# Kernel optimization log

Measured on AMD Instinct MI355X. Metric: run time of the kernel, lower is better.

The kernel has to match this reference:

```python
import jax, jax.numpy as jnp
import numpy as np

N = 4096    # channels * n = 4 * 1024
N_IN = 1024
FC = 512


def ldr_layer(x, G, H, subd_A, subd_B, bias):
    """y = W x + bias, where W = sum_i K(A, g_i) K(B, h_i)^T and A, B are
    subdiagonal matrices with entries subd_A, subd_B (Krylov LDR fast multiply).

    Closed form: K(A, g)[i, j] = g[i-j] * c[i] / c[i-j] for i >= j (0 otherwise),
    with c = [1, cumprod(subd_A)]. This turns the multiply into FFT
    correlations/convolutions of length 2n instead of a dense n x n GEMM.
    x: (b, n); G, H: (r, n); subd_A, subd_B: (n-1,); bias: (n,).
    """
    n = x.shape[-1]
    one = jnp.ones((1,), x.dtype)
    c = jnp.concatenate([one, jnp.cumprod(subd_A)])   # (n,) cumulative subdiag products of A
    d = jnp.concatenate([one, jnp.cumprod(subd_B)])   # (n,)
    L = 2 * n
    q = H / d                                          # (r, n)
    gp = G / c                                         # (r, n)
    p = x * d                                          # (b, n)
    # u[b, r, j] = (K(B, h_r)^T x)[j] = sum_k q[r, k] * p[b, j + k]  (cross-correlation)
    Fp = jnp.fft.rfft(p, n=L)                          # (b, n+1)
    Fq = jnp.fft.rfft(q, n=L)                          # (r, n+1)
    u = jnp.fft.irfft(Fp[:, None] * jnp.conj(Fq)[None], n=L)[..., :n]  # (b, r, n)
    # out[b, i] = c[i] * sum_r (gp_r * u[b, r])_conv[i]  (causal convolution)
    Fg = jnp.fft.rfft(gp, n=L)                         # (r, n+1)
    Fu = jnp.fft.rfft(u, n=L)                          # (b, r, n+1)
    out = jnp.fft.irfft(jnp.einsum('rk,brk->bk', Fg, Fu), n=L)[:, :n]
    return c * out + bias


def setup_inputs() -> dict:
    key = jax.random.key(0)
    ks = jax.random.split(key, 14)
    std = 0.01  # params.init_stddev
    f32 = jnp.float32
    inp = {
        'x': jax.random.normal(ks[0], (128, N_IN), f32),
        'G1': std * jax.random.normal(ks[1], (48, N), f32),
        'H1': std * jax.random.normal(ks[2], (48, N), f32),
        'subd_A1': jnp.exp(0.01 * jax.random.normal(ks[3], (N - 1,), f32)),
        'subd_B1': jnp.exp(0.01 * jax.random.normal(ks[4], (N - 1,), f32)),
        'b1': std * jax.random.normal(ks[5], (N,), f32),
        'G2': std * jax.random.normal(ks[6], (16, N), f32),
        'H2': std * jax.random.normal(ks[7], (16, N), f32),
        'subd_A2': jnp.exp(0.01 * jax.random.normal(ks[8], (N - 1,), f32)),
        'subd_B2': jnp.exp(0.01 * jax.random.normal(ks[9], (N - 1,), f32)),
        'b2': std * jax.random.normal(ks[10], (N,), f32),
        'W_logits': jax.random.normal(ks[11], (10, FC), f32) / np.sqrt(FC).astype(np.float32),
        'b_logits': std * jax.random.normal(ks[12], (10,), f32),
    }
    return inp


def reference(x, G1, H1, subd_A1, subd_B1, b1, G2, H2, subd_A2, subd_B2, b2,
              W_logits, b_logits):
    bsz, n_in = x.shape
    xp = jnp.concatenate([x, jnp.zeros((bsz, N - n_in), x.dtype)], axis=-1)  # pad to channels*n
    h = jax.nn.relu(ldr_layer(xp, G1, H1, subd_A1, subd_B1, b1))
    h = jax.nn.relu(ldr_layer(h, G2, H2, subd_A2, subd_B2, b2))
    return h[:, :FC] @ W_logits.T + b_logits
```

## Files before the change

### kernel.cpp

```cpp
#include <hip/hip_runtime.h>
#include <hip/hip_bf16.h>

#define BATCH 128
#define NIN   1024
#define NFULL 4096
#define R1    48
#define R2    16
#define FCDIM 512
#define NOUT  10

#define WS_C1  0
#define WS_D1  4096
#define WS_C2  8192
#define WS_D2  12288
#define WS_Q1  16384
#define WS_GP1 (WS_Q1 + R1*NFULL)
#define WS_Q2  (WS_GP1 + R1*NFULL)
#define WS_GP2 (WS_Q2 + R2*NFULL)
#define WS_P1  (WS_GP2 + R2*NFULL)
#define WS_P2  (WS_P1 + BATCH*NIN)
#define WS_H2  (WS_P2 + BATCH*NFULL)
#define WS_PT1 (WS_H2 + BATCH*FCDIM)
#define WS_P2M (WS_PT1 + NIN*NFULL)
#define WS_CT1 (WS_P2M + FCDIM*NFULL)
#define WS_CT2 (WS_CT1 + 16*5120)
#define WS_VP1 (WS_CT2 + 8*4608)
#define WS_VP2 (WS_VP1 + 4*BATCH*NFULL)
#define WS_END (WS_VP2 + 32*BATCH*FCDIM)

#define NCH1 16
#define NCH2 8
#define CHROWS 64
#define CTLD1 5120
#define CTLD2 4608

typedef __attribute__((ext_vector_type(8))) short bf16x8;
typedef __attribute__((ext_vector_type(4))) float f32x4;

__device__ __forceinline__ unsigned short f2b(float f) {
    unsigned u = __builtin_bit_cast(unsigned, f);
    return (unsigned short)((u + 0x7fffu + ((u >> 16) & 1u)) >> 16);
}
__device__ __forceinline__ float b2f(unsigned short h) {
    unsigned u = ((unsigned)h) << 16;
    return __builtin_bit_cast(float, u);
}
#define MFMA16(a, b, c) __builtin_amdgcn_mfma_f32_16x16x32_bf16(a, b, c, 0, 0, 0)

__global__ void __launch_bounds__(256) prep_fused(
    const float* __restrict__ x, const float* __restrict__ G1,
    const float* __restrict__ H1, const float* __restrict__ G2,
    const float* __restrict__ H2, const float* __restrict__ sA1,
    const float* __restrict__ sB1, const float* __restrict__ sA2,
    const float* __restrict__ sB2, float* __restrict__ ws) {
    __shared__ float cd[4096];
    __shared__ float tot[256];
    int b = blockIdx.x, t = threadIdx.x;
    const float* src;
    int kind, r;
    if (b < 48)       { kind = 0; r = b;       src = sB1; }
    else if (b < 96)  { kind = 1; r = b - 48;  src = sA1; }
    else if (b < 112) { kind = 2; r = b - 96;  src = sB2; }
    else if (b < 128) { kind = 3; r = b - 112; src = sA2; }
    else              { kind = 4; r = b - 128; src = sB1; }
    float loc[16];
    float prod = 1.f;
#pragma unroll
    for (int u = 0; u < 16; ++u) {
        int idx = t * 16 + u;
        float e = (idx == 0) ? 1.f : src[idx - 1];
        prod *= e;
        loc[u] = prod;
    }
    tot[t] = prod;
    __syncthreads();
    for (int off = 1; off < 256; off <<= 1) {
        float v = (t >= off) ? tot[t - off] : 1.f;
        __syncthreads();
        tot[t] *= v;
        __syncthreads();
    }
    float excl = (t == 0) ? 1.f : tot[t - 1];
#pragma unroll
    for (int u = 0; u < 16; ++u) cd[t * 16 + u] = excl * loc[u];
    __syncthreads();

    if (kind == 0) {
        const float* s0 = H1 + (size_t)r * NFULL;
        float* dst = ws + WS_Q1 + (size_t)r * NFULL;
#pragma unroll
        for (int u = 0; u < 16; ++u) { int i = t + u * 256; dst[i] = s0[i] / cd[i]; }
        if (r == 0) { float* d1 = ws + WS_D1;
#pragma unroll
            for (int u = 0; u < 16; ++u) { int i = t + u * 256; d1[i] = cd[i]; } }
    } else if (kind == 1) {
        const float* s0 = G1 + (size_t)r * NFULL;
        float* dst = ws + WS_GP1 + (size_t)r * NFULL;
#pragma unroll
        for (int u = 0; u < 16; ++u) { int i = t + u * 256; dst[i] = s0[i] / cd[i]; }
        if (r == 0) { float* c1 = ws + WS_C1;
#pragma unroll
            for (int u = 0; u < 16; ++u) { int i = t + u * 256; c1[i] = cd[i]; } }
    } else if (kind == 2) {
        const float* s0 = H2 + (size_t)r * NFULL;
        float* dst = ws + WS_Q2 + (size_t)r * NFULL;
#pragma unroll
        for (int u = 0; u < 16; ++u) { int i = t + u * 256; dst[i] = s0[i] / cd[i]; }
        if (r == 0) { float* d2 = ws + WS_D2;
#pragma unroll
            for (int u = 0; u < 16; ++u) { int i = t + u * 256; d2[i] = cd[i]; } }
    } else if (kind == 3) {
        const float* s0 = G2 + (size_t)r * NFULL;
        float* dst = ws + WS_GP2 + (size_t)r * NFULL;
#pragma unroll
        for (int u = 0; u < 16; ++u) { int i = t + u * 256; dst[i] = s0[i] / cd[i]; }
        if (r == 0) { float* c2 = ws + WS_C2;
#pragma unroll
            for (int u = 0; u < 16; ++u) { int i = t + u * 256; c2[i] = cd[i]; } }
    } else {
        unsigned short* p1h = (unsigned short*)(ws + WS_P1);
        unsigned short* p1l = p1h + BATCH * NIN;
        int row0 = r * 4;
#pragma unroll
        for (int u = 0; u < 16; ++u) {
            int lin = t + u * 256;
            int row = row0 + (lin >> 10), col = lin & 1023;
            float f = x[(size_t)row * NIN + col] * cd[col];
            unsigned short h = f2b(f);
            p1h[(size_t)row * NIN + col] = h;
            p1l[(size_t)row * NIN + col] = f2b(f - b2f(h));
        }
    }
}

__global__ void __launch_bounds__(256) gemm_rank_kernel(float* __restrict__ ws) {
    const int which = blockIdx.z;
    if (which == 1 && blockIdx.y >= 8) return;
    const float* A = ws + (which == 0 ? WS_Q1  : WS_GP2);
    const float* B = ws + (which == 0 ? WS_GP1 : WS_Q2);
    float* C       = ws + (which == 0 ? WS_PT1 : WS_P2M);
    const int Kr   = which == 0 ? R1 : R2;
    __shared__ float As[R1 * 68];
    __shared__ float Bs[R1 * 68];
    int tid = threadIdx.x;
    int tx = tid & 15, ty = tid >> 4;
    int n0 = blockIdx.x * 64;
    int m0 = blockIdx.y * 64;
    int nf4 = Kr * 16;
    for (int lin = tid; lin < nf4; lin += 256) {
        int r = lin >> 4, i4 = lin & 15;
        *(float4*)&As[r * 68 + i4 * 4] = *(const float4*)&A[(size_t)r * NFULL + m0 + i4 * 4];
        *(float4*)&Bs[r * 68 + i4 * 4] = *(const float4*)&B[(size_t)r * NFULL + n0 + i4 * 4];
    }
    __syncthreads();
    float acc[4][4] = {};
#pragma unroll 8
    for (int r = 0; r < Kr; ++r) {
        float4 a4 = *(const float4*)&As[r * 68 + ty * 4];
        float4 b4 = *(const float4*)&Bs[r * 68 + tx * 4];
        acc[0][0] += a4.x * b4.x; acc[0][1] += a4.x * b4.y;
        acc[0][2] += a4.x * b4.z; acc[0][3] += a4.x * b4.w;
        acc[1][0] += a4.y * b4.x; acc[1][1] += a4.y * b4.y;
        acc[1][2] += a4.y * b4.z; acc[1][3] += a4.y * b4.w;
        acc[2][0] += a4.z * b4.x; acc[2][1] += a4.z * b4.y;
        acc[2][2] += a4.z * b4.z; acc[2][3] += a4.z * b4.w;
        acc[3][0] += a4.w * b4.x; acc[3][1] += a4.w * b4.y;
        acc[3][2] += a4.w * b4.z; acc[3][3] += a4.w * b4.w;
    }
#pragma unroll
    for (int i = 0; i < 4; ++i) {
        int m = m0 + ty * 4 + i;
        *(float4*)&C[(size_t)m * NFULL + n0 + tx * 4] =
            make_float4(acc[i][0], acc[i][1], acc[i][2], acc[i][3]);
    }
}

__global__ void diag_scan_p1(float* __restrict__ ws) {
    const int which = blockIdx.z;
    const int nch   = which == 0 ? NCH1 : NCH2;
    if (blockIdx.y >= (unsigned)nch) return;
    float* P        = ws + (which == 0 ? WS_PT1 : WS_P2M);
    float* ctot     = ws + (which == 0 ? WS_CT1 : WS_CT2);
    const int R     = which == 0 ? NIN : FCDIM;
    const int nd    = R + NFULL - 1;
    const int ctld  = which == 0 ? CTLD1 : CTLD2;
    int t = blockIdx.x * 256 + threadIdx.x;
    if (t >= nd) return;
    int doff = t - (R - 1);
    int z = blockIdx.y;
    int m0 = z * CHROWS;
    int mlo = max(m0, -doff);
    int mhi = min(m0 + CHROWS, min(NFULL - doff, R));
    float run = 0.f;
    if (mlo < mhi) {
        float* p = P + (size_t)mlo * NFULL + (mlo + doff);
        const size_t step = NFULL + 1;
        int len = mhi - mlo;
        int s = 0;
        for (; s + 16 <= len; s += 16) {
            float v[16];
#pragma unroll
            for (int u = 0; u < 16; ++u) v[u] = p[u * step];
#pragma unroll
            for (int u = 0; u < 16; ++u) { run += v[u]; v[u] = run; }
#pragma unroll
            for (int u = 0; u < 16; ++u) p[u * step] = v[u];
            p += 16 * step;
        }
        for (; s < len; ++s) { float v = *p; run += v; *p = run; p += step; }
    }
    ctot[(size_t)z * ctld + t] = run;
}

__global__ void off_prefix(float* __restrict__ ws) {
    const int which = blockIdx.z;
    float* ct      = ws + (which == 0 ? WS_CT1 : WS_CT2);
    const int ctld = which == 0 ? CTLD1 : CTLD2;
    const int nch  = which == 0 ? NCH1 : NCH2;
    int t = blockIdx.x * 256 + threadIdx.x;
    if (t >= ctld) return;
    float run = 0.f;
    for (int z = 0; z < nch; ++z) {
        float v = ct[(size_t)z * ctld + t];
        ct[(size_t)z * ctld + t] = run;
        run += v;
    }
}

#define L1_LOADA(H0, H1, L0, L1v, KS) { \
    int kk_ = kbase + (KS) * 32 + 8 * g; \
    const unsigned short* pa_ = p1h + (size_t)(mq * 32 + lm) * NIN + kk_; \
    const unsigned short* pb_ = p1l + (size_t)(mq * 32 + lm) * NIN + kk_; \
    H0 = *(const bf16x8*)pa_;  H1 = *(const bf16x8*)(pa_ + 16 * NIN); \
    L0 = *(const bf16x8*)pb_;  L1v = *(const bf16x8*)(pb_ + 16 * NIN); }

#define L1_LOADS(KS) { \
    int kg_ = kbase + (KS) * 32 + 2 * k2; \
    const float* pr_ = P1 + (size_t)kg_ * NFULL + n0 + 2 * n2; \
    float2 va_ = *(const float2*)pr_; \
    float2 vb_ = *(const float2*)(pr_ + NFULL); \
    const float* orow_ = OFF1 + (size_t)(kg_ >> 6) * CTLD1 + (1023 + n0 + 2 * n2 - kg_); \
    float om_ = orow_[-1], oc_ = orow_[0], op_ = orow_[1]; \
    f00 = va_.x + oc_; f01 = va_.y + op_; f10 = vb_.x + om_; f11 = vb_.y + oc_; }

#define L1_WRITES() { \
    unsigned short h00_ = f2b(f00), h10_ = f2b(f10), h01_ = f2b(f01), h11_ = f2b(f11); \
    int a0_ = (2 * n2) * 20 + k2; \
    Bh[a0_]      = (unsigned)h00_ | ((unsigned)h10_ << 16); \
    Bh[a0_ + 20] = (unsigned)h01_ | ((unsigned)h11_ << 16); \
    Bl[a0_]      = (unsigned)f2b(f00 - b2f(h00_)) | ((unsigned)f2b(f10 - b2f(h10_)) << 16); \
    Bl[a0_ + 20] = (unsigned)f2b(f01 - b2f(h01_)) | ((unsigned)f2b(f11 - b2f(h11_)) << 16); }

#define L1_COMPUTE(H0, H1, L0, L1v) { \
    int nb_ = (nh * 32 + lm) * 20 + 4 * g; \
    uint4 uh0_ = *(const uint4*)&Bh[nb_];       uint4 ul0_ = *(const uint4*)&Bl[nb_]; \
    uint4 uh1_ = *(const uint4*)&Bh[nb_ + 320]; uint4 ul1_ = *(const uint4*)&Bl[nb_ + 320]; \
    bf16x8 bh0_ = __builtin_bit_cast(bf16x8, uh0_), bl0_ = __builtin_bit_cast(bf16x8, ul0_); \
    bf16x8 bh1_ = __builtin_bit_cast(bf16x8, uh1_), bl1_ = __builtin_bit_cast(bf16x8, ul1_); \
    acc00 = MFMA16(H0, bh0_, acc00); acc10 = MFMA16(H1, bh0_, acc10); \
    acc01 = MFMA16(H0, bh1_, acc01); acc11 = MFMA16(H1, bh1_, acc11); \
    acc00 = MFMA16(H0, bl0_, acc00); acc10 = MFMA16(H1, bl0_, acc10); \
    acc01 = MFMA16(H0, bl1_, acc01); acc11 = MFMA16(H1, bl1_, acc11); \
    acc00 = MFMA16(L0, bh0_, acc00); acc10 = MFMA16(L1v, bh0_, acc10); \
    acc01 = MFMA16(L0, bh1_, acc01); acc11 = MFMA16(L1v, bh1_, acc11); }

#define L1_STEP(CH0, CH1, CL0, CL1, NH0, NH1, NL0, NL1, KS, LAST) \
    __syncthreads(); \
    L1_WRITES(); \
    if (!(LAST)) { L1_LOADS((KS) + 1); L1_LOADA(NH0, NH1, NL0, NL1, (KS) + 1); } \
    __syncthreads(); \
    L1_COMPUTE(CH0, CH1, CL0, CL1);

__global__ void __launch_bounds__(512)
gemm2_l1_mfma(const float* __restrict__ P1, const float* __restrict__ OFF1,
              const unsigned short* __restrict__ p1h,
              const unsigned short* __restrict__ p1l, float* __restrict__ vp) {
    __shared__ unsigned Bh[64 * 20];
    __shared__ unsigned Bl[64 * 20];
    const int t = threadIdx.x;
    const int n0 = blockIdx.x * 64;
    const int kbase = blockIdx.z * 256;
    const int w = t >> 6, l = t & 63;
    const int mq = w >> 1, nh = w & 1;
    const int lm = l & 15, g = l >> 4;
    const int k2 = t >> 5, n2 = t & 31;

    f32x4 zero = {0.f, 0.f, 0.f, 0.f};
    f32x4 acc00 = zero, acc01 = zero, acc10 = zero, acc11 = zero;
    bf16x8 ahA0, ahA1, alA0, alA1, ahB0, ahB1, alB0, alB1;
    float f00, f01, f10, f11;

    L1_LOADS(0);
    L1_LOADA(ahA0, ahA1, alA0, alA1, 0);
    L1_STEP(ahA0, ahA1, alA0, alA1, ahB0, ahB1, alB0, alB1, 0, 0)
    L1_STEP(ahB0, ahB1, alB0, alB1, ahA0, ahA1, alA0, alA1, 1, 0)
    L1_STEP(ahA0, ahA1, alA0, alA1, ahB0, ahB1, alB0, alB1, 2, 0)
    L1_STEP(ahB0, ahB1, alB0, alB1, ahA0, ahA1, alA0, alA1, 3, 0)
    L1_STEP(ahA0, ahA1, alA0, alA1, ahB0, ahB1, alB0, alB1, 4, 0)
    L1_STEP(ahB0, ahB1, alB0, alB1, ahA0, ahA1, alA0, alA1, 5, 0)
    L1_STEP(ahA0, ahA1, alA0, alA1, ahB0, ahB1, alB0, alB1, 6, 0)
    L1_STEP(ahB0, ahB1, alB0, alB1, ahA0, ahA1, alA0, alA1, 7, 1)

    float* dst = vp + (size_t)blockIdx.z * BATCH * NFULL;
    int row0 = mq * 32 + 4 * g;
    int col0 = n0 + nh * 32 + lm;
#pragma unroll
    for (int r = 0; r < 4; ++r) {
        dst[(size_t)(row0 + r) * NFULL + col0]           = acc00[r];
        dst[(size_t)(row0 + r) * NFULL + col0 + 16]      = acc01[r];
        dst[(size_t)(row0 + 16 + r) * NFULL + col0]      = acc10[r];
        dst[(size_t)(row0 + 16 + r) * NFULL + col0 + 16] = acc11[r];
    }
}

__global__ void reduce_l1_kernel(const float* __restrict__ vp, const float* __restrict__ c1,
                                 const float* __restrict__ b1, const float* __restrict__ d2,
                                 unsigned short* __restrict__ p2h,
                                 unsigned short* __restrict__ p2l) {
    int idx4 = blockIdx.x * 256 + threadIdx.x;
    int base = idx4 * 4;
    int n = base & (NFULL - 1);
    float4 s = make_float4(0.f, 0.f, 0.f, 0.f);
#pragma unroll
    for (int z = 0; z < 4; ++z) {
        float4 v = *(const float4*)&vp[(size_t)z * BATCH * NFULL + base];
        s.x += v.x; s.y += v.y; s.z += v.z; s.w += v.w;
    }
    float4 cc = *(const float4*)&c1[n];
    float4 bb = *(const float4*)&b1[n];
    float4 dd = *(const float4*)&d2[n];
    float f[4];
    f[0] = fmaxf(cc.x * s.x + bb.x, 0.f) * dd.x;
    f[1] = fmaxf(cc.y * s.y + bb.y, 0.f) * dd.y;
    f[2] = fmaxf(cc.z * s.z + bb.z, 0.f) * dd.z;
    f[3] = fmaxf(cc.w * s.w + bb.w, 0.f) * dd.w;
    ushort4 hv, lv;
    unsigned short h;
    h = f2b(f[0]); hv.x = h; lv.x = f2b(f[0] - b2f(h));
    h = f2b(f[1]); hv.y = h; lv.y = f2b(f[1] - b2f(h));
    h = f2b(f[2]); hv.z = h; lv.z = f2b(f[2] - b2f(h));
    h = f2b(f[3]); hv.w = h; lv.w = f2b(f[3] - b2f(h));
    *(ushort4*)&p2h[base] = hv;
    *(ushort4*)&p2l[base] = lv;
}

__global__ void __launch_bounds__(512)
gemm2_l2_mfma(const unsigned short* __restrict__ p2h,
              const unsigned short* __restrict__ p2l,
              const float* __restrict__ M2, const float* __restrict__ OFF2,
              float* __restrict__ vp) {
    const int t = threadIdx.x;
    const int n0 = blockIdx.x * 64;
    const int kbase = blockIdx.z * 128;
    const int w = t >> 6, l = t & 63;
    const int mq = w >> 1, nh = w & 1;
    const int lm = l & 15, g = l >> 4;
    f32x4 zero = {0.f, 0.f, 0.f, 0.f};
    f32x4 acc00 = zero, acc01 = zero, acc10 = zero, acc11 = zero;
    const int nn0 = n0 + nh * 32 + lm;
    const int nn1 = nn0 + 16;
    const float* om0 = OFF2 + (size_t)(nn0 >> 6) * CTLD2 + (511 - nn0);
    const float* om1 = OFF2 + (size_t)(nn1 >> 6) * CTLD2 + (511 - nn1);
#pragma unroll
    for (int ks = 0; ks < 4; ++ks) {
        int kk = kbase + ks * 32 + 8 * g;
        const unsigned short* pa = p2h + (size_t)(mq * 32 + lm) * NFULL + kk;
        const unsigned short* pb = p2l + (size_t)(mq * 32 + lm) * NFULL + kk;
        bf16x8 ah0 = *(const bf16x8*)pa, ah1 = *(const bf16x8*)(pa + 16 * NFULL);
        bf16x8 al0 = *(const bf16x8*)pb, al1 = *(const bf16x8*)(pb + 16 * NFULL);
        bf16x8 bh0, bl0, bh1, bl1;
        {
            const float* pm = M2 + (size_t)nn0 * NFULL + kk;
#pragma unroll
            for (int r = 0; r < 8; ++r) {
                float f = pm[r] + om0[kk + r];
                unsigned short h = f2b(f);
                bh0[r] = (short)h; bl0[r] = (short)f2b(f - b2f(h));
            }
        }
        {
            const float* pm = M2 + (size_t)nn1 * NFULL + kk;
#pragma unroll
            for (int r = 0; r < 8; ++r) {
                float f = pm[r] + om1[kk + r];
                unsigned short h = f2b(f);
                bh1[r] = (short)h; bl1[r] = (short)f2b(f - b2f(h));
            }
        }
        acc00 = MFMA16(ah0, bh0, acc00); acc10 = MFMA16(ah1, bh0, acc10);
        acc01 = MFMA16(ah0, bh1, acc01); acc11 = MFMA16(ah1, bh1, acc11);
        acc00 = MFMA16(ah0, bl0, acc00); acc10 = MFMA16(ah1, bl0, acc10);
        acc01 = MFMA16(ah0, bl1, acc01); acc11 = MFMA16(ah1, bl1, acc11);
        acc00 = MFMA16(al0, bh0, acc00); acc10 = MFMA16(al1, bh0, acc10);
        acc01 = MFMA16(al0, bh1, acc01); acc11 = MFMA16(al1, bh1, acc11);
    }
    float* dst = vp + (size_t)blockIdx.z * BATCH * FCDIM;
    int row0 = mq * 32 + 4 * g;
    int col0 = n0 + nh * 32 + lm;
#pragma unroll
    for (int r = 0; r < 4; ++r) {
        dst[(size_t)(row0 + r) * FCDIM + col0]           = acc00[r];
        dst[(size_t)(row0 + r) * FCDIM + col0 + 16]      = acc01[r];
        dst[(size_t)(row0 + 16 + r) * FCDIM + col0]      = acc10[r];
        dst[(size_t)(row0 + 16 + r) * FCDIM + col0 + 16] = acc11[r];
    }
}

__global__ void fused_out_kernel(const float* __restrict__ vp, const float* __restrict__ c2,
                                 const float* __restrict__ b2, const float* __restrict__ Wl,
                                 const float* __restrict__ bl, float* __restrict__ out) {
    __shared__ float h2s[FCDIM];
    int b = blockIdx.x, t = threadIdx.x;
    for (int col = t; col < FCDIM; col += 256) {
        float s = 0.f;
#pragma unroll
        for (int z = 0; z < 32; ++z)
            s += vp[((size_t)z * BATCH + b) * FCDIM + col];
        h2s[col] = fmaxf(c2[col] * s + b2[col], 0.f);
    }
    __syncthreads();
    int w = t >> 6, lane = t & 63;
    for (int o = w; o < NOUT; o += 4) {
        float s = 0.f;
#pragma unroll
        for (int i = lane; i < FCDIM; i += 64) s += h2s[i] * Wl[(size_t)o * FCDIM + i];
#pragma unroll
        for (int off = 32; off > 0; off >>= 1) s += __shfl_down(s, off);
        if (lane == 0) out[(size_t)b * NOUT + o] = s + bl[o];
    }
}

extern "C" void kernel_launch(void* const* d_in, const int* in_sizes, int n_in,
                              void* d_out, int out_size, void* d_ws, size_t ws_size,
                              hipStream_t stream) {
    const float* x   = (const float*)d_in[0];
    const float* G1  = (const float*)d_in[1];
    const float* H1  = (const float*)d_in[2];
    const float* sA1 = (const float*)d_in[3];
    const float* sB1 = (const float*)d_in[4];
    const float* b1  = (const float*)d_in[5];
    const float* G2  = (const float*)d_in[6];
    const float* H2  = (const float*)d_in[7];
    const float* sA2 = (const float*)d_in[8];
    const float* sB2 = (const float*)d_in[9];
    const float* b2  = (const float*)d_in[10];
    const float* Wl  = (const float*)d_in[11];
    const float* bl  = (const float*)d_in[12];
    float* out = (float*)d_out;
    float* ws = (float*)d_ws;
    (void)in_sizes; (void)n_in; (void)out_size; (void)ws_size;

    unsigned short* p1h = (unsigned short*)(ws + WS_P1);
    unsigned short* p1l = p1h + BATCH * NIN;
    unsigned short* p2h = (unsigned short*)(ws + WS_P2);
    unsigned short* p2l = p2h + BATCH * NFULL;

    prep_fused<<<160, 256, 0, stream>>>(x, G1, H1, G2, H2, sA1, sB1, sA2, sB2, ws);

    gemm_rank_kernel<<<dim3(64, 16, 2), 256, 0, stream>>>(ws);

    diag_scan_p1<<<dim3(20, NCH1, 2), 256, 0, stream>>>(ws);
    off_prefix<<<dim3(20, 1, 2), 256, 0, stream>>>(ws);

    gemm2_l1_mfma<<<dim3(64, 1, 4), 512, 0, stream>>>(ws + WS_PT1, ws + WS_CT1,
                                                      p1h, p1l, ws + WS_VP1);
    reduce_l1_kernel<<<512, 256, 0, stream>>>(ws + WS_VP1, ws + WS_C1, b1, ws + WS_D2,
                                              p2h, p2l);

    gemm2_l2_mfma<<<dim3(8, 1, 32), 512, 0, stream>>>(p2h, p2l, ws + WS_P2M,
                                                      ws + WS_CT2, ws + WS_VP2);

    fused_out_kernel<<<BATCH, 256, 0, stream>>>(ws + WS_VP2, ws + WS_C2, b2, Wl, bl, out);
}
```

Before: 70.94 us.

## Fuse rank-factor scaling into GEMM, drop layer-1 split-K, prefetch layer-2 operands

```diff
diff --git a/kernel.cpp b/kernel.cpp
--- a/kernel.cpp
+++ b/kernel.cpp
@@ -13,24 +13,18 @@
 #define WS_D1  4096
 #define WS_C2  8192
 #define WS_D2  12288
-#define WS_Q1  16384
-#define WS_GP1 (WS_Q1 + R1*NFULL)
-#define WS_Q2  (WS_GP1 + R1*NFULL)
-#define WS_GP2 (WS_Q2 + R2*NFULL)
-#define WS_P1  (WS_GP2 + R2*NFULL)
+#define WS_P1  16384
 #define WS_P2  (WS_P1 + BATCH*NIN)
-#define WS_H2  (WS_P2 + BATCH*NFULL)
-#define WS_PT1 (WS_H2 + BATCH*FCDIM)
+#define WS_PT1 (WS_P2 + BATCH*NFULL)
 #define WS_P2M (WS_PT1 + NIN*NFULL)
 #define WS_CT1 (WS_P2M + FCDIM*NFULL)
-#define WS_CT2 (WS_CT1 + 16*5120)
-#define WS_VP1 (WS_CT2 + 8*4608)
-#define WS_VP2 (WS_VP1 + 4*BATCH*NFULL)
-#define WS_END (WS_VP2 + 32*BATCH*FCDIM)
-
-#define NCH1 16
-#define NCH2 8
-#define CHROWS 64
+#define WS_CT2 (WS_CT1 + 32*5120)
+#define WS_VP2 (WS_CT2 + 16*4608)
+#define WS_END (WS_VP2 + 16*BATCH*FCDIM)
+
+#define NCH1 32
+#define NCH2 16
+#define CHROWS 32
 #define CTLD1 5120
 #define CTLD2 4608
 
@@ -48,21 +42,14 @@
 #define MFMA16(a, b, c) __builtin_amdgcn_mfma_f32_16x16x32_bf16(a, b, c, 0, 0, 0)
 
 __global__ void __launch_bounds__(256) prep_fused(
-    const float* __restrict__ x, const float* __restrict__ G1,
-    const float* __restrict__ H1, const float* __restrict__ G2,
-    const float* __restrict__ H2, const float* __restrict__ sA1,
+    const float* __restrict__ x, const float* __restrict__ sA1,
     const float* __restrict__ sB1, const float* __restrict__ sA2,
     const float* __restrict__ sB2, float* __restrict__ ws) {
     __shared__ float cd[4096];
     __shared__ float tot[256];
     int b = blockIdx.x, t = threadIdx.x;
-    const float* src;
-    int kind, r;
-    if (b < 48)       { kind = 0; r = b;       src = sB1; }
-    else if (b < 96)  { kind = 1; r = b - 48;  src = sA1; }
-    else if (b < 112) { kind = 2; r = b - 96;  src = sB2; }
-    else if (b < 128) { kind = 3; r = b - 112; src = sA2; }
-    else              { kind = 4; r = b - 128; src = sB1; }
+    const float* src = (b == 0) ? sA1 : (b == 1) ? sB1 : (b == 2) ? sA2
+                      : (b == 3) ? sB2 : sB1;
     float loc[16];
     float prod = 1.f;
 #pragma unroll
@@ -85,42 +72,14 @@
     for (int u = 0; u < 16; ++u) cd[t * 16 + u] = excl * loc[u];
     __syncthreads();
 
-    if (kind == 0) {
-        const float* s0 = H1 + (size_t)r * NFULL;
-        float* dst = ws + WS_Q1 + (size_t)r * NFULL;
-#pragma unroll
-        for (int u = 0; u < 16; ++u) { int i = t + u * 256; dst[i] = s0[i] / cd[i]; }
-        if (r == 0) { float* d1 = ws + WS_D1;
-#pragma unroll
-            for (int u = 0; u < 16; ++u) { int i = t + u * 256; d1[i] = cd[i]; } }
-    } else if (kind == 1) {
-        const float* s0 = G1 + (size_t)r * NFULL;
-        float* dst = ws + WS_GP1 + (size_t)r * NFULL;
-#pragma unroll
-        for (int u = 0; u < 16; ++u) { int i = t + u * 256; dst[i] = s0[i] / cd[i]; }
-        if (r == 0) { float* c1 = ws + WS_C1;
-#pragma unroll
-            for (int u = 0; u < 16; ++u) { int i = t + u * 256; c1[i] = cd[i]; } }
-    } else if (kind == 2) {
-        const float* s0 = H2 + (size_t)r * NFULL;
-        float* dst = ws + WS_Q2 + (size_t)r * NFULL;
-#pragma unroll
-        for (int u = 0; u < 16; ++u) { int i = t + u * 256; dst[i] = s0[i] / cd[i]; }
-        if (r == 0) { float* d2 = ws + WS_D2;
-#pragma unroll
-            for (int u = 0; u < 16; ++u) { int i = t + u * 256; d2[i] = cd[i]; } }
-    } else if (kind == 3) {
-        const float* s0 = G2 + (size_t)r * NFULL;
-        float* dst = ws + WS_GP2 + (size_t)r * NFULL;
-#pragma unroll
-        for (int u = 0; u < 16; ++u) { int i = t + u * 256; dst[i] = s0[i] / cd[i]; }
-        if (r == 0) { float* c2 = ws + WS_C2;
-#pragma unroll
-            for (int u = 0; u < 16; ++u) { int i = t + u * 256; c2[i] = cd[i]; } }
+    if (b < 4) {
+        float* dst = ws + (size_t)b * 4096;
+#pragma unroll
+        for (int u = 0; u < 16; ++u) { int i = t + u * 256; dst[i] = cd[i]; }
     } else {
         unsigned short* p1h = (unsigned short*)(ws + WS_P1);
         unsigned short* p1l = p1h + BATCH * NIN;
-        int row0 = r * 4;
+        int row0 = (b - 4) * 4;
 #pragma unroll
         for (int u = 0; u < 16; ++u) {
             int lin = t + u * 256;
@@ -133,13 +92,18 @@
     }
 }
 
-__global__ void __launch_bounds__(256) gemm_rank_kernel(float* __restrict__ ws) {
+__global__ void __launch_bounds__(256) gemm_rank_kernel(
+    const float* __restrict__ H1, const float* __restrict__ G1,
+    const float* __restrict__ G2, const float* __restrict__ H2,
+    float* __restrict__ ws) {
     const int which = blockIdx.z;
     if (which == 1 && blockIdx.y >= 8) return;
-    const float* A = ws + (which == 0 ? WS_Q1  : WS_GP2);
-    const float* B = ws + (which == 0 ? WS_GP1 : WS_Q2);
-    float* C       = ws + (which == 0 ? WS_PT1 : WS_P2M);
-    const int Kr   = which == 0 ? R1 : R2;
+    const float* A    = which == 0 ? H1 : G2;
+    const float* B    = which == 0 ? G1 : H2;
+    const float* divA = ws + (which == 0 ? WS_D1 : WS_C2);
+    const float* divB = ws + (which == 0 ? WS_C1 : WS_D2);
+    float* C          = ws + (which == 0 ? WS_PT1 : WS_P2M);
+    const int Kr      = which == 0 ? R1 : R2;
     __shared__ float As[R1 * 68];
     __shared__ float Bs[R1 * 68];
     int tid = threadIdx.x;
@@ -149,8 +113,14 @@
     int nf4 = Kr * 16;
     for (int lin = tid; lin < nf4; lin += 256) {
         int r = lin >> 4, i4 = lin & 15;
-        *(float4*)&As[r * 68 + i4 * 4] = *(const float4*)&A[(size_t)r * NFULL + m0 + i4 * 4];
-        *(float4*)&Bs[r * 68 + i4 * 4] = *(const float4*)&B[(size_t)r * NFULL + n0 + i4 * 4];
+        float4 va = *(const float4*)&A[(size_t)r * NFULL + m0 + i4 * 4];
+        float4 da = *(const float4*)&divA[m0 + i4 * 4];
+        va.x /= da.x; va.y /= da.y; va.z /= da.z; va.w /= da.w;
+        *(float4*)&As[r * 68 + i4 * 4] = va;
+        float4 vb = *(const float4*)&B[(size_t)r * NFULL + n0 + i4 * 4];
+        float4 db = *(const float4*)&divB[n0 + i4 * 4];
+        vb.x /= db.x; vb.y /= db.y; vb.z /= db.z; vb.w /= db.w;
+        *(float4*)&Bs[r * 68 + i4 * 4] = vb;
     }
     __syncthreads();
     float acc[4][4] = {};
@@ -228,18 +198,18 @@
 }
 
 #define L1_LOADA(H0, H1, L0, L1v, KS) { \
-    int kk_ = kbase + (KS) * 32 + 8 * g; \
+    int kk_ = (KS) * 32 + 8 * g; \
     const unsigned short* pa_ = p1h + (size_t)(mq * 32 + lm) * NIN + kk_; \
     const unsigned short* pb_ = p1l + (size_t)(mq * 32 + lm) * NIN + kk_; \
     H0 = *(const bf16x8*)pa_;  H1 = *(const bf16x8*)(pa_ + 16 * NIN); \
     L0 = *(const bf16x8*)pb_;  L1v = *(const bf16x8*)(pb_ + 16 * NIN); }
 
 #define L1_LOADS(KS) { \
-    int kg_ = kbase + (KS) * 32 + 2 * k2; \
+    int kg_ = (KS) * 32 + 2 * k2; \
     const float* pr_ = P1 + (size_t)kg_ * NFULL + n0 + 2 * n2; \
     float2 va_ = *(const float2*)pr_; \
     float2 vb_ = *(const float2*)(pr_ + NFULL); \
-    const float* orow_ = OFF1 + (size_t)(kg_ >> 6) * CTLD1 + (1023 + n0 + 2 * n2 - kg_); \
+    const float* orow_ = OFF1 + (size_t)(kg_ >> 5) * CTLD1 + (1023 + n0 + 2 * n2 - kg_); \
     float om_ = orow_[-1], oc_ = orow_[0], op_ = orow_[1]; \
     f00 = va_.x + oc_; f01 = va_.y + op_; f10 = vb_.x + om_; f11 = vb_.y + oc_; }
 
@@ -264,22 +234,17 @@
     acc00 = MFMA16(L0, bh0_, acc00); acc10 = MFMA16(L1v, bh0_, acc10); \
     acc01 = MFMA16(L0, bh1_, acc01); acc11 = MFMA16(L1v, bh1_, acc11); }
 
-#define L1_STEP(CH0, CH1, CL0, CL1, NH0, NH1, NL0, NL1, KS, LAST) \
-    __syncthreads(); \
-    L1_WRITES(); \
-    if (!(LAST)) { L1_LOADS((KS) + 1); L1_LOADA(NH0, NH1, NL0, NL1, (KS) + 1); } \
-    __syncthreads(); \
-    L1_COMPUTE(CH0, CH1, CL0, CL1);
-
 __global__ void __launch_bounds__(512)
 gemm2_l1_mfma(const float* __restrict__ P1, const float* __restrict__ OFF1,
               const unsigned short* __restrict__ p1h,
-              const unsigned short* __restrict__ p1l, float* __restrict__ vp) {
+              const unsigned short* __restrict__ p1l,
+              const float* __restrict__ c1, const float* __restrict__ b1,
+              const float* __restrict__ d2,
+              unsigned short* __restrict__ p2h, unsigned short* __restrict__ p2l) {
     __shared__ unsigned Bh[64 * 20];
     __shared__ unsigned Bl[64 * 20];
     const int t = threadIdx.x;
     const int n0 = blockIdx.x * 64;
-    const int kbase = blockIdx.z * 256;
     const int w = t >> 6, l = t & 63;
     const int mq = w >> 1, nh = w & 1;
     const int lm = l & 15, g = l >> 4;
@@ -292,56 +257,44 @@
 
     L1_LOADS(0);
     L1_LOADA(ahA0, ahA1, alA0, alA1, 0);
-    L1_STEP(ahA0, ahA1, alA0, alA1, ahB0, ahB1, alB0, alB1, 0, 0)
-    L1_STEP(ahB0, ahB1, alB0, alB1, ahA0, ahA1, alA0, alA1, 1, 0)
-    L1_STEP(ahA0, ahA1, alA0, alA1, ahB0, ahB1, alB0, alB1, 2, 0)
-    L1_STEP(ahB0, ahB1, alB0, alB1, ahA0, ahA1, alA0, alA1, 3, 0)
-    L1_STEP(ahA0, ahA1, alA0, alA1, ahB0, ahB1, alB0, alB1, 4, 0)
-    L1_STEP(ahB0, ahB1, alB0, alB1, ahA0, ahA1, alA0, alA1, 5, 0)
-    L1_STEP(ahA0, ahA1, alA0, alA1, ahB0, ahB1, alB0, alB1, 6, 0)
-    L1_STEP(ahB0, ahB1, alB0, alB1, ahA0, ahA1, alA0, alA1, 7, 1)
-
-    float* dst = vp + (size_t)blockIdx.z * BATCH * NFULL;
+    for (int it = 0; it < 16; ++it) {
+        int ks = 2 * it;
+        __syncthreads();
+        L1_WRITES();
+        L1_LOADS(ks + 1);
+        L1_LOADA(ahB0, ahB1, alB0, alB1, ks + 1);
+        __syncthreads();
+        L1_COMPUTE(ahA0, ahA1, alA0, alA1);
+        __syncthreads();
+        L1_WRITES();
+        if (ks + 1 < 31) {
+            L1_LOADS(ks + 2);
+            L1_LOADA(ahA0, ahA1, alA0, alA1, ks + 2);
+        }
+        __syncthreads();
+        L1_COMPUTE(ahB0, ahB1, alB0, alB1);
+    }
+
     int row0 = mq * 32 + 4 * g;
     int col0 = n0 + nh * 32 + lm;
+    float cc0 = c1[col0], bb0 = b1[col0], dd0 = d2[col0];
+    float cc1 = c1[col0 + 16], bb1 = b1[col0 + 16], dd1 = d2[col0 + 16];
 #pragma unroll
     for (int r = 0; r < 4; ++r) {
-        dst[(size_t)(row0 + r) * NFULL + col0]           = acc00[r];
-        dst[(size_t)(row0 + r) * NFULL + col0 + 16]      = acc01[r];
-        dst[(size_t)(row0 + 16 + r) * NFULL + col0]      = acc10[r];
-        dst[(size_t)(row0 + 16 + r) * NFULL + col0 + 16] = acc11[r];
-    }
-}
-
-__global__ void reduce_l1_kernel(const float* __restrict__ vp, const float* __restrict__ c1,
-                                 const float* __restrict__ b1, const float* __restrict__ d2,
-                                 unsigned short* __restrict__ p2h,
-                                 unsigned short* __restrict__ p2l) {
-    int idx4 = blockIdx.x * 256 + threadIdx.x;
-    int base = idx4 * 4;
-    int n = base & (NFULL - 1);
-    float4 s = make_float4(0.f, 0.f, 0.f, 0.f);
-#pragma unroll
-    for (int z = 0; z < 4; ++z) {
-        float4 v = *(const float4*)&vp[(size_t)z * BATCH * NFULL + base];
-        s.x += v.x; s.y += v.y; s.z += v.z; s.w += v.w;
-    }
-    float4 cc = *(const float4*)&c1[n];
-    float4 bb = *(const float4*)&b1[n];
-    float4 dd = *(const float4*)&d2[n];
-    float f[4];
-    f[0] = fmaxf(cc.x * s.x + bb.x, 0.f) * dd.x;
-    f[1] = fmaxf(cc.y * s.y + bb.y, 0.f) * dd.y;
-    f[2] = fmaxf(cc.z * s.z + bb.z, 0.f) * dd.z;
-    f[3] = fmaxf(cc.w * s.w + bb.w, 0.f) * dd.w;
-    ushort4 hv, lv;
-    unsigned short h;
-    h = f2b(f[0]); hv.x = h; lv.x = f2b(f[0] - b2f(h));
-    h = f2b(f[1]); hv.y = h; lv.y = f2b(f[1] - b2f(h));
-    h = f2b(f[2]); hv.z = h; lv.z = f2b(f[2] - b2f(h));
-    h = f2b(f[3]); hv.w = h; lv.w = f2b(f[3] - b2f(h));
-    *(ushort4*)&p2h[base] = hv;
-    *(ushort4*)&p2l[base] = lv;
+        float f; unsigned short h; size_t idx;
+        idx = (size_t)(row0 + r) * NFULL + col0;
+        f = fmaxf(cc0 * acc00[r] + bb0, 0.f) * dd0;
+        h = f2b(f); p2h[idx] = h; p2l[idx] = f2b(f - b2f(h));
+        idx = (size_t)(row0 + r) * NFULL + col0 + 16;
+        f = fmaxf(cc1 * acc01[r] + bb1, 0.f) * dd1;
+        h = f2b(f); p2h[idx] = h; p2l[idx] = f2b(f - b2f(h));
+        idx = (size_t)(row0 + 16 + r) * NFULL + col0;
+        f = fmaxf(cc0 * acc10[r] + bb0, 0.f) * dd0;
+        h = f2b(f); p2h[idx] = h; p2l[idx] = f2b(f - b2f(h));
+        idx = (size_t)(row0 + 16 + r) * NFULL + col0 + 16;
+        f = fmaxf(cc1 * acc11[r] + bb1, 0.f) * dd1;
+        h = f2b(f); p2h[idx] = h; p2l[idx] = f2b(f - b2f(h));
+    }
 }
 
 __global__ void __launch_bounds__(512)
@@ -351,7 +304,7 @@
               float* __restrict__ vp) {
     const int t = threadIdx.x;
     const int n0 = blockIdx.x * 64;
-    const int kbase = blockIdx.z * 128;
+    const int kbase = blockIdx.z * 256;
     const int w = t >> 6, l = t & 63;
     const int mq = w >> 1, nh = w & 1;
     const int lm = l & 15, g = l >> 4;
@@ -359,33 +312,43 @@
     f32x4 acc00 = zero, acc01 = zero, acc10 = zero, acc11 = zero;
     const int nn0 = n0 + nh * 32 + lm;
     const int nn1 = nn0 + 16;
-    const float* om0 = OFF2 + (size_t)(nn0 >> 6) * CTLD2 + (511 - nn0);
-    const float* om1 = OFF2 + (size_t)(nn1 >> 6) * CTLD2 + (511 - nn1);
-#pragma unroll
-    for (int ks = 0; ks < 4; ++ks) {
+    const float* om0 = OFF2 + (size_t)(nn0 >> 5) * CTLD2 + (511 - nn0);
+    const float* om1 = OFF2 + (size_t)(nn1 >> 5) * CTLD2 + (511 - nn1);
+    const float* pm0 = M2 + (size_t)nn0 * NFULL;
+    const float* pm1 = M2 + (size_t)nn1 * NFULL;
+
+    float4 c0a, c0b, c1a, c1b, x0a, x0b, x1a, x1b;
+    {
+        int kk = kbase + 8 * g;
+        c0a = *(const float4*)&pm0[kk]; c0b = *(const float4*)&pm0[kk + 4];
+        c1a = *(const float4*)&pm1[kk]; c1b = *(const float4*)&pm1[kk + 4];
+    }
+#pragma unroll
+    for (int ks = 0; ks < 8; ++ks) {
         int kk = kbase + ks * 32 + 8 * g;
+        if (ks < 7) {
+            int kn = kk + 32;
+            x0a = *(const float4*)&pm0[kn]; x0b = *(const float4*)&pm0[kn + 4];
+            x1a = *(const float4*)&pm1[kn]; x1b = *(const float4*)&pm1[kn + 4];
+        }
         const unsigned short* pa = p2h + (size_t)(mq * 32 + lm) * NFULL + kk;
         const unsigned short* pb = p2l + (size_t)(mq * 32 + lm) * NFULL + kk;
         bf16x8 ah0 = *(const bf16x8*)pa, ah1 = *(const bf16x8*)(pa + 16 * NFULL);
         bf16x8 al0 = *(const bf16x8*)pb, al1 = *(const bf16x8*)(pb + 16 * NFULL);
         bf16x8 bh0, bl0, bh1, bl1;
-        {
-            const float* pm = M2 + (size_t)nn0 * NFULL + kk;
-#pragma unroll
-            for (int r = 0; r < 8; ++r) {
-                float f = pm[r] + om0[kk + r];
-                unsigned short h = f2b(f);
-                bh0[r] = (short)h; bl0[r] = (short)f2b(f - b2f(h));
-            }
-        }
-        {
-            const float* pm = M2 + (size_t)nn1 * NFULL + kk;
-#pragma unroll
-            for (int r = 0; r < 8; ++r) {
-                float f = pm[r] + om1[kk + r];
-                unsigned short h = f2b(f);
-                bh1[r] = (short)h; bl1[r] = (short)f2b(f - b2f(h));
-            }
+        float m0v[8] = {c0a.x, c0a.y, c0a.z, c0a.w, c0b.x, c0b.y, c0b.z, c0b.w};
+        float m1v[8] = {c1a.x, c1a.y, c1a.z, c1a.w, c1b.x, c1b.y, c1b.z, c1b.w};
+#pragma unroll
+        for (int r = 0; r < 8; ++r) {
+            float f = m0v[r] + om0[kk + r];
+            unsigned short h = f2b(f);
+            bh0[r] = (short)h; bl0[r] = (short)f2b(f - b2f(h));
+        }
+#pragma unroll
+        for (int r = 0; r < 8; ++r) {
+            float f = m1v[r] + om1[kk + r];
+            unsigned short h = f2b(f);
+            bh1[r] = (short)h; bl1[r] = (short)f2b(f - b2f(h));
         }
         acc00 = MFMA16(ah0, bh0, acc00); acc10 = MFMA16(ah1, bh0, acc10);
         acc01 = MFMA16(ah0, bh1, acc01); acc11 = MFMA16(ah1, bh1, acc11);
@@ -393,6 +356,7 @@
         acc01 = MFMA16(ah0, bl1, acc01); acc11 = MFMA16(ah1, bl1, acc11);
         acc00 = MFMA16(al0, bh0, acc00); acc10 = MFMA16(al1, bh0, acc10);
         acc01 = MFMA16(al0, bh1, acc01); acc11 = MFMA16(al1, bh1, acc11);
+        c0a = x0a; c0b = x0b; c1a = x1a; c1b = x1b;
     }
     float* dst = vp + (size_t)blockIdx.z * BATCH * FCDIM;
     int row0 = mq * 32 + 4 * g;
@@ -414,7 +378,7 @@
     for (int col = t; col < FCDIM; col += 256) {
         float s = 0.f;
 #pragma unroll
-        for (int z = 0; z < 32; ++z)
+        for (int z = 0; z < 16; ++z)
             s += vp[((size_t)z * BATCH + b) * FCDIM + col];
         h2s[col] = fmaxf(c2[col] * s + b2[col], 0.f);
     }
@@ -455,19 +419,18 @@
     unsigned short* p2h = (unsigned short*)(ws + WS_P2);
     unsigned short* p2l = p2h + BATCH * NFULL;
 
-    prep_fused<<<160, 256, 0, stream>>>(x, G1, H1, G2, H2, sA1, sB1, sA2, sB2, ws);
-
-    gemm_rank_kernel<<<dim3(64, 16, 2), 256, 0, stream>>>(ws);
+    prep_fused<<<36, 256, 0, stream>>>(x, sA1, sB1, sA2, sB2, ws);
+
+    gemm_rank_kernel<<<dim3(64, 16, 2), 256, 0, stream>>>(H1, G1, G2, H2, ws);
 
     diag_scan_p1<<<dim3(20, NCH1, 2), 256, 0, stream>>>(ws);
     off_prefix<<<dim3(20, 1, 2), 256, 0, stream>>>(ws);
 
-    gemm2_l1_mfma<<<dim3(64, 1, 4), 512, 0, stream>>>(ws + WS_PT1, ws + WS_CT1,
-                                                      p1h, p1l, ws + WS_VP1);
-    reduce_l1_kernel<<<512, 256, 0, stream>>>(ws + WS_VP1, ws + WS_C1, b1, ws + WS_D2,
-                                              p2h, p2l);
-
-    gemm2_l2_mfma<<<dim3(8, 1, 32), 512, 0, stream>>>(p2h, p2l, ws + WS_P2M,
+    gemm2_l1_mfma<<<dim3(64, 1, 1), 512, 0, stream>>>(ws + WS_PT1, ws + WS_CT1,
+                                                      p1h, p1l, ws + WS_C1, b1,
+                                                      ws + WS_D2, p2h, p2l);
+
+    gemm2_l2_mfma<<<dim3(8, 1, 16), 512, 0, stream>>>(p2h, p2l, ws + WS_P2M,
                                                       ws + WS_CT2, ws + WS_VP2);
 
     fused_out_kernel<<<BATCH, 256, 0, stream>>>(ws + WS_VP2, ws + WS_C2, b2, Wl, bl, out);
```

Measured after the change: 105.9 us. 49.2% more time.
